# Optimization experiments

Measured on AMD Instinct MI355X. Metric: run time of the kernel, lower is better.

## Reference

```python
import jax, jax.numpy as jnp
import numpy as np

STRIDE = 4.0
NUM_CLASSES = 3
GH, GW = 40, 60
NBOX = 2 * GH * GW  # 4800
OBJ_CONF = 0.5
NMS_CONF = 0.4
# flattened anchor vector per cell after source's stack/transpose/tile/reshape:
# [wide_w, tall_w, wide_h, tall_h] (in grid units)
ANCH = jnp.array([60.0, 30.0, 20.0, 40.0], dtype=jnp.float32)


def _conv(x, w, b):
    y = jax.lax.conv_general_dilated(x, w, (1, 1), 'VALID',
                                     dimension_numbers=('NHWC', 'HWIO', 'NHWC'))
    return jax.nn.relu(y + b)


def _pool(x):
    return jax.lax.reduce_window(x, -jnp.inf, jax.lax.max,
                                 (1, 2, 2, 1), (1, 2, 2, 1), 'VALID')


def _predict_transform(p):
    # p: [B, GH, GW, 16]
    gx, gy = jnp.meshgrid(jnp.arange(GW, dtype=p.dtype), jnp.arange(GH, dtype=p.dtype))
    off = jnp.stack([gx, gy], axis=-1)  # [GH, GW, 2]
    xy1 = (jax.nn.sigmoid(p[..., 0:2]) + off) * STRIDE
    wh1 = jnp.exp(p[..., 2:4]) * ANCH[:2] * STRIDE
    conf1 = jax.nn.sigmoid(p[..., 4:5])
    cls1 = jax.nn.sigmoid(p[..., 5:8])
    xy2 = (p[..., 8:10] + off) * STRIDE          # source: no sigmoid on box2 xy
    wh2 = jnp.exp(p[..., 10:12]) * ANCH[2:4] * STRIDE
    conf2 = p[..., 12:13]                         # source: box2 conf never sigmoided
    cls2 = jax.nn.sigmoid(p[..., 13:16])
    return jnp.concatenate([xy1, wh1, conf1, cls1, xy2, wh2, conf2, cls2], axis=-1)


def _iou_one_vs_all(b, B):
    # b: [8], B: [N,8]; boxes are (cx, cy, w, h, ...). +1 pixel convention as in source.
    bx1, by1 = b[0] - b[2] / 2, b[1] - b[3] / 2
    bx2, by2 = b[0] + b[2] / 2, b[1] + b[3] / 2
    Bx1, By1 = B[:, 0] - B[:, 2] / 2, B[:, 1] - B[:, 3] / 2
    Bx2, By2 = B[:, 0] + B[:, 2] / 2, B[:, 1] + B[:, 3] / 2
    iw = jnp.clip(jnp.minimum(bx2, Bx2) - jnp.maximum(bx1, Bx1) + 1, 0)
    ih = jnp.clip(jnp.minimum(by2, By2) - jnp.maximum(by1, By1) + 1, 0)
    inter = iw * ih
    a1 = (bx2 - bx1 + 1) * (by2 - by1 + 1)
    a2 = (Bx2 - Bx1 + 1) * (By2 - By1 + 1)
    return inter / (a1 + a2 - inter)


def _nms_class(boxes, mask):
    # boxes: [N, 8], mask: [N] bool -> keep mask [N] bool in original order
    n = boxes.shape[0]
    score = jnp.where(mask, boxes[:, 4], -1.0)
    order = jnp.argsort(-score)               # confidence-descending
    bs = boxes[order]
    keep0 = mask[order]
    idx = jnp.arange(n)

    def body(i, keep):
        ious = _iou_one_vs_all(bs[i], bs)
        sup = (ious >= NMS_CONF) & (idx > i) & keep[i]
        return keep & ~sup

    keep = jax.lax.fori_loop(0, n, body, keep0)
    return jnp.zeros_like(mask).at[order].set(keep)


def _filter_boxes(pred_img):
    # pred_img: [GH, GW, 16] -> keep mask [NUM_CLASSES, NBOX]
    b1 = pred_img[..., :8].reshape(-1, 8)
    b2 = pred_img[..., 8:].reshape(-1, 8)
    boxes = jnp.concatenate([b1, b2], axis=0)  # [NBOX, 8]
    valid = boxes[:, 4] > OBJ_CONF
    cls_idx = jnp.argmax(boxes[:, 5:5 + NUM_CLASSES], axis=1)
    masks = valid[None, :] & (cls_idx[None, :] == jnp.arange(NUM_CLASSES)[:, None])
    return jax.vmap(lambda m: _nms_class(boxes, m))(masks)


def setup_inputs() -> dict:
    key = jax.random.key(0)
    ks = jax.random.split(key, 8)
    B = 8
    img = jax.random.normal(ks[0], (B, 160, 240, 3), dtype=jnp.float32)
    w1 = jax.random.normal(ks[1], (6, 6, 3, 32), dtype=jnp.float32) * 0.05
    b1 = jnp.zeros((32,), jnp.float32)
    w2 = jax.random.normal(ks[2], (3, 3, 32, 64), dtype=jnp.float32) * 0.05
    b2 = jnp.zeros((64,), jnp.float32)
    w3 = jax.random.normal(ks[3], (3, 3, 64, 128), dtype=jnp.float32) * 0.05
    b3 = jnp.zeros((128,), jnp.float32)
    F = 35 * 55 * 128  # flattened backbone features
    wd1 = jax.random.normal(ks[4], (F, 256), dtype=jnp.float32) * 0.01
    bd1 = jnp.zeros((256,), jnp.float32)
    wd2 = jax.random.normal(ks[5], (256, GH * GW * 16), dtype=jnp.float32) * 0.02
    bd2 = jnp.zeros((GH * GW * 16,), jnp.float32)
    return {'img': img, 'w1': w1, 'b1': b1, 'w2': w2, 'b2': b2, 'w3': w3, 'b3': b3,
            'wd1': wd1, 'bd1': bd1, 'wd2': wd2, 'bd2': bd2}


def reference(img, w1, b1, w2, b2, w3, b3, wd1, bd1, wd2, bd2):
    x = _conv(img, w1, b1)      # [B,155,235,32]
    x = _pool(x)                # [B,77,117,32]
    x = _conv(x, w2, b2)        # [B,75,115,64]
    x = _pool(x)                # [B,37,57,64]
    x = _conv(x, w3, b3)        # [B,35,55,128]
    x = x.reshape(x.shape[0], -1)
    x = jax.nn.relu(x @ wd1 + bd1)   # dropout is identity at inference
    x = x @ wd2 + bd2
    x = x.reshape(-1, GH, GW, 16)
    pred = _predict_transform(x)             # [B, GH, GW, 16]
    keep = jax.vmap(_filter_boxes)(pred)     # [B, NUM_CLASSES, NBOX] bool
    return pred, keep
```

## Files before the change

kernel.cpp:

```cpp
#include <hip/hip_runtime.h>
#include <stdint.h>


static __device__ __forceinline__ float sigmoidf_(float x) {
  return 1.0f / (1.0f + expf(-x));
}

__global__ __launch_bounds__(256) void k_conv1p(const float* __restrict__ in,
    const float* __restrict__ w, const float* __restrict__ bias, float* __restrict__ out) {
  __shared__ float s_in[21 * 37 * 3];
  __shared__ float s_w[6 * 6 * 3 * 32];
  int tx = blockIdx.x, ty = blockIdx.y, n = blockIdx.z;
  int tid = threadIdx.x;
  int iy0 = ty * 16, ix0 = tx * 32;
  for (int idx = tid; idx < 3456; idx += 256) s_w[idx] = w[idx];
  for (int idx = tid; idx < 21 * 37 * 3; idx += 256) {
    int c = idx % 3;
    int rem = idx / 3;
    int x = rem % 37, y = rem / 37;
    int gy = iy0 + y, gx = ix0 + x;
    float v = 0.f;
    if (gy < 160 && gx < 240) v = in[((size_t)(n * 160 + gy) * 240 + gx) * 3 + c];
    s_in[idx] = v;
  }
  __syncthreads();

  int cg = tid >> 6;
  int l = tid & 63;
  int py = l >> 2;
  int px0 = (l & 3) * 8;

  float acc[8][8];
  float bj[8];
#pragma unroll
  for (int j = 0; j < 8; j++) bj[j] = bias[cg * 8 + j];
#pragma unroll
  for (int k = 0; k < 8; k++)
#pragma unroll
    for (int j = 0; j < 8; j++) acc[k][j] = bj[j];

#pragma unroll 1
  for (int ky = 0; ky < 6; ky++) {
#pragma unroll 1
    for (int kx = 0; kx < 6; kx++) {
#pragma unroll 1
      for (int c = 0; c < 3; c++) {
        const float* ib = s_in + ((py + ky) * 37 + px0 + kx) * 3 + c;
        float iv[8];
#pragma unroll
        for (int k = 0; k < 8; k++) iv[k] = ib[k * 3];
        const float* wb = s_w + ((ky * 6 + kx) * 3 + c) * 32 + cg * 8;
        float wv[8];
#pragma unroll
        for (int j = 0; j < 8; j++) wv[j] = wb[j];
#pragma unroll
        for (int k = 0; k < 8; k++)
#pragma unroll
          for (int j = 0; j < 8; j++) acc[k][j] = fmaf(iv[k], wv[j], acc[k][j]);
      }
    }
  }
  float pm[4][8];
#pragma unroll
  for (int kk = 0; kk < 4; kk++)
#pragma unroll
    for (int j = 0; j < 8; j++) pm[kk][j] = fmaxf(acc[2 * kk][j], acc[2 * kk + 1][j]);
#pragma unroll
  for (int kk = 0; kk < 4; kk++)
#pragma unroll
    for (int j = 0; j < 8; j++) {
      float o = __shfl_down(pm[kk][j], 4);
      pm[kk][j] = fmaxf(pm[kk][j], o);
    }
  if (!(py & 1)) {
    int pyp = ty * 8 + (py >> 1);
    if (pyp < 77) {
#pragma unroll
      for (int kk = 0; kk < 4; kk++) {
        int pxp = tx * 16 + (l & 3) * 4 + kk;
        if (pxp < 117) {
          float* op = out + ((size_t)(n * 77 + pyp) * 117 + pxp) * 32 + cg * 8;
          float4 v0, v1;
          v0.x = fmaxf(pm[kk][0], 0.f); v0.y = fmaxf(pm[kk][1], 0.f);
          v0.z = fmaxf(pm[kk][2], 0.f); v0.w = fmaxf(pm[kk][3], 0.f);
          v1.x = fmaxf(pm[kk][4], 0.f); v1.y = fmaxf(pm[kk][5], 0.f);
          v1.z = fmaxf(pm[kk][6], 0.f); v1.w = fmaxf(pm[kk][7], 0.f);
          ((float4*)op)[0] = v0;
          ((float4*)op)[1] = v1;
        }
      }
    }
  }
}

__global__ __launch_bounds__(256) void k_conv2p(const float* __restrict__ in,
    const float* __restrict__ w, const float* __restrict__ bias, float* __restrict__ out) {
  __shared__ float s_in[32 * 10 * 18];
  int tx = blockIdx.x, ty = blockIdx.y, n = blockIdx.z;
  int tid = threadIdx.x;
  int iy0 = ty * 8, ix0 = tx * 16;
  for (int idx = tid; idx < 10 * 18 * 32; idx += 256) {
    int c = idx & 31;
    int rem = idx >> 5;
    int x = rem % 18, y = rem / 18;
    int gy = iy0 + y, gx = ix0 + x;
    float v = 0.f;
    if (gy < 77 && gx < 117) v = in[((size_t)(n * 77 + gy) * 117 + gx) * 32 + c];
    s_in[c * 180 + y * 18 + x] = v;
  }
  __syncthreads();

  int cg = tid >> 4;
  int pg = tid & 15;
  int py = pg >> 1;
  int px0 = (pg & 1) * 8;

  float acc[8][4];
  float bj[4];
#pragma unroll
  for (int j = 0; j < 4; j++) bj[j] = bias[cg * 4 + j];
#pragma unroll
  for (int k = 0; k < 8; k++)
#pragma unroll
    for (int j = 0; j < 4; j++) acc[k][j] = bj[j];

#pragma unroll 1
  for (int ky = 0; ky < 3; ky++) {
#pragma unroll 1
    for (int kx = 0; kx < 3; kx++) {
      const float* wbase = w + (size_t)((ky * 3 + kx) * 32) * 64 + cg * 4;
      const float* ibase = s_in + (py + ky) * 18 + px0 + kx;
#pragma unroll 4
      for (int c = 0; c < 32; c++) {
        float4 wa = *(const float4*)(wbase + (size_t)c * 64);
        const float* ib = ibase + c * 180;
        float iv[8];
#pragma unroll
        for (int k = 0; k < 8; k++) iv[k] = ib[k];
#pragma unroll
        for (int k = 0; k < 8; k++) {
          acc[k][0] = fmaf(iv[k], wa.x, acc[k][0]);
          acc[k][1] = fmaf(iv[k], wa.y, acc[k][1]);
          acc[k][2] = fmaf(iv[k], wa.z, acc[k][2]);
          acc[k][3] = fmaf(iv[k], wa.w, acc[k][3]);
        }
      }
    }
  }
  float pm[4][4];
#pragma unroll
  for (int kk = 0; kk < 4; kk++)
#pragma unroll
    for (int j = 0; j < 4; j++) pm[kk][j] = fmaxf(acc[2 * kk][j], acc[2 * kk + 1][j]);
#pragma unroll
  for (int kk = 0; kk < 4; kk++)
#pragma unroll
    for (int j = 0; j < 4; j++) {
      float o = __shfl_down(pm[kk][j], 2);
      pm[kk][j] = fmaxf(pm[kk][j], o);
    }
  if (!(pg & 2)) {
    int pyp = ty * 4 + (py >> 1);
    if (pyp < 37) {
#pragma unroll
      for (int kk = 0; kk < 4; kk++) {
        int pxp = tx * 8 + (pg & 1) * 4 + kk;
        if (pxp < 57) {
          float* op = out + ((size_t)(n * 37 + pyp) * 57 + pxp) * 64 + cg * 4;
          float4 v0;
          v0.x = fmaxf(pm[kk][0], 0.f); v0.y = fmaxf(pm[kk][1], 0.f);
          v0.z = fmaxf(pm[kk][2], 0.f); v0.w = fmaxf(pm[kk][3], 0.f);
          ((float4*)op)[0] = v0;
        }
      }
    }
  }
}

__global__ __launch_bounds__(256) void k_conv3(const float* __restrict__ in,
    const float* __restrict__ w, const float* __restrict__ bias, float* __restrict__ out) {
  __shared__ float s_in[64 * 6 * 18];
  int tx = blockIdx.x, ty = blockIdx.y, z = blockIdx.z;
  int n = z >> 1, h = z & 1;
  int tid = threadIdx.x;
  int iy0 = ty * 4, ix0 = tx * 16;
  for (int idx = tid; idx < 6 * 18 * 64; idx += 256) {
    int c = idx & 63;
    int rem = idx >> 6;
    int x = rem % 18, y = rem / 18;
    int gy = iy0 + y, gx = ix0 + x;
    float v = 0.f;
    if (gy < 37 && gx < 57) v = in[((size_t)(n * 37 + gy) * 57 + gx) * 64 + c];
    s_in[c * 108 + y * 18 + x] = v;
  }
  __syncthreads();

  int cg = tid >> 4;
  int pg = tid & 15;
  int py = pg >> 2;
  int px0 = (pg & 3) * 4;
  int ob = h * 64 + cg * 4;

  float acc[4][4];
  float bj[4];
#pragma unroll
  for (int j = 0; j < 4; j++) bj[j] = bias[ob + j];
#pragma unroll
  for (int k = 0; k < 4; k++)
#pragma unroll
    for (int j = 0; j < 4; j++) acc[k][j] = bj[j];

#pragma unroll 1
  for (int ky = 0; ky < 3; ky++) {
#pragma unroll 1
    for (int kx = 0; kx < 3; kx++) {
      const float* wbase = w + (size_t)((ky * 3 + kx) * 64) * 128 + ob;
      const float* ibase = s_in + (py + ky) * 18 + px0 + kx;
#pragma unroll 4
      for (int c = 0; c < 64; c++) {
        float4 wa = *(const float4*)(wbase + (size_t)c * 128);
        const float* ib = ibase + c * 108;
        float iv[4];
#pragma unroll
        for (int k = 0; k < 4; k++) iv[k] = ib[k];
#pragma unroll
        for (int k = 0; k < 4; k++) {
          acc[k][0] = fmaf(iv[k], wa.x, acc[k][0]);
          acc[k][1] = fmaf(iv[k], wa.y, acc[k][1]);
          acc[k][2] = fmaf(iv[k], wa.z, acc[k][2]);
          acc[k][3] = fmaf(iv[k], wa.w, acc[k][3]);
        }
      }
    }
  }
  int oy = iy0 + py;
  if (oy < 35) {
#pragma unroll
    for (int k = 0; k < 4; k++) {
      int ox = ix0 + px0 + k;
      if (ox < 55) {
        float* op = out + ((size_t)(n * 35 + oy) * 55 + ox) * 128 + ob;
        float4 v0;
        v0.x = fmaxf(acc[k][0], 0.f); v0.y = fmaxf(acc[k][1], 0.f);
        v0.z = fmaxf(acc[k][2], 0.f); v0.w = fmaxf(acc[k][3], 0.f);
        ((float4*)op)[0] = v0;
      }
    }
  }
}

__global__ __launch_bounds__(256) void k_dense1(const float* __restrict__ a3,
    const float* __restrict__ wd1, float* __restrict__ part) {
  __shared__ float red[4][64][33];
  __shared__ float s_x[256][8];
  int c = blockIdx.x;
  int tid = threadIdx.x;
  int c4 = tid & 63;
  int ks = tid >> 6;
  int k0 = c * 256;
  int kn = 246400 - k0;
  if (kn > 256) kn = 256;
  for (int idx = tid; idx < 2048; idx += 256) {
    int nn = idx >> 8, r = idx & 255;
    int rr = k0 + r;
    if (rr > 246399) rr = 246399;
    s_x[r][nn] = a3[(size_t)nn * 246400 + rr];
  }
  __syncthreads();
  float acc[8][4];
#pragma unroll
  for (int n = 0; n < 8; n++)
#pragma unroll
    for (int j = 0; j < 4; j++) acc[n][j] = 0.f;
  int kbeg = ks * 64;
  int kend = kbeg + 64;
  if (kend > kn) kend = kn;
#pragma unroll 8
  for (int kk = kbeg; kk < kend; kk++) {
    float4 wv = *(const float4*)(wd1 + (size_t)(k0 + kk) * 256 + c4 * 4);
    float4 xa = *(const float4*)&s_x[kk][0];
    float4 xb = *(const float4*)&s_x[kk][4];
    float xs[8] = {xa.x, xa.y, xa.z, xa.w, xb.x, xb.y, xb.z, xb.w};
#pragma unroll
    for (int n = 0; n < 8; n++) {
      acc[n][0] = fmaf(xs[n], wv.x, acc[n][0]);
      acc[n][1] = fmaf(xs[n], wv.y, acc[n][1]);
      acc[n][2] = fmaf(xs[n], wv.z, acc[n][2]);
      acc[n][3] = fmaf(xs[n], wv.w, acc[n][3]);
    }
  }
#pragma unroll
  for (int n = 0; n < 8; n++)
#pragma unroll
    for (int j = 0; j < 4; j++) red[ks][c4][n * 4 + j] = acc[n][j];
  __syncthreads();
  for (int o = tid; o < 2048; o += 256) {
    int col = o & 255, n = o >> 8;
    int cc = col >> 2, j = col & 3;
    float s = red[0][cc][n * 4 + j] + red[1][cc][n * 4 + j] +
              red[2][cc][n * 4 + j] + red[3][cc][n * 4 + j];
    part[(size_t)c * 2048 + n * 256 + col] = s;
  }
}

__global__ __launch_bounds__(256) void k_reduce1a(const float* __restrict__ part,
    float* __restrict__ partr) {
  int bx = blockIdx.x;
  int t = blockIdx.y * 256 + threadIdx.x;
  int cbeg = bx * 61;
  int cend = cbeg + 61;
  if (cend > 963) cend = 963;
  float s = 0.f;
#pragma unroll 4
  for (int c = cbeg; c < cend; c++) s += part[(size_t)c * 2048 + t];
  partr[(size_t)bx * 2048 + t] = s;
}

__global__ __launch_bounds__(256) void k_dense2t(const float* __restrict__ partr,
    const float* __restrict__ bd1, const float* __restrict__ wd2,
    const float* __restrict__ bd2, float* __restrict__ pred,
    float4* __restrict__ boxd4, float* __restrict__ meta) {
  __shared__ float red[8][32][33];
  __shared__ float s_d1[256][8];
  int jb = blockIdx.x;
  int tid = threadIdx.x;
  for (int idx = tid; idx < 2048; idx += 256) {
    int n = idx >> 8, j = idx & 255;
    float s = 0.f;
#pragma unroll
    for (int b = 0; b < 16; b++) s += partr[b * 2048 + idx];
    s_d1[j][n] = fmaxf(s + bd1[j], 0.f);
  }
  __syncthreads();
  int c4 = tid & 31;
  int ks = tid >> 5;
  int j0 = jb * 128 + c4 * 4;
  float acc[8][4];
#pragma unroll
  for (int n = 0; n < 8; n++)
#pragma unroll
    for (int j = 0; j < 4; j++) acc[n][j] = 0.f;
#pragma unroll 4
  for (int kk = 0; kk < 32; kk++) {
    int row = ks * 32 + kk;
    float4 wv = *(const float4*)(wd2 + (size_t)row * 38400 + j0);
    float4 xa = *(const float4*)&s_d1[row][0];
    float4 xb = *(const float4*)&s_d1[row][4];
    float xs[8] = {xa.x, xa.y, xa.z, xa.w, xb.x, xb.y, xb.z, xb.w};
#pragma unroll
    for (int n = 0; n < 8; n++) {
      acc[n][0] = fmaf(xs[n], wv.x, acc[n][0]);
      acc[n][1] = fmaf(xs[n], wv.y, acc[n][1]);
      acc[n][2] = fmaf(xs[n], wv.z, acc[n][2]);
      acc[n][3] = fmaf(xs[n], wv.w, acc[n][3]);
    }
  }
#pragma unroll
  for (int n = 0; n < 8; n++)
#pragma unroll
    for (int j = 0; j < 4; j++) red[ks][c4][n * 4 + j] = acc[n][j];
  __syncthreads();
  if (tid >= 64) return;
  int n = tid >> 3, cc = tid & 7;
  int cell = jb * 8 + cc;
  float v[16];
#pragma unroll
  for (int q = 0; q < 16; q++) {
    int lc = cc * 16 + q;
    int cq = lc >> 2, jq = lc & 3;
    float s = 0.f;
#pragma unroll
    for (int g = 0; g < 8; g++) s += red[g][cq][n * 4 + jq];
    v[q] = s + bd2[jb * 128 + lc];
  }
  float gx = (float)(cell % 60), gy = (float)(cell / 60);
  float o[16];
  o[0] = (sigmoidf_(v[0]) + gx) * 4.0f;
  o[1] = (sigmoidf_(v[1]) + gy) * 4.0f;
  o[2] = expf(v[2]) * 60.0f * 4.0f;
  o[3] = expf(v[3]) * 30.0f * 4.0f;
  o[4] = sigmoidf_(v[4]);
  o[5] = sigmoidf_(v[5]);
  o[6] = sigmoidf_(v[6]);
  o[7] = sigmoidf_(v[7]);
  o[8] = (v[8] + gx) * 4.0f;
  o[9] = (v[9] + gy) * 4.0f;
  o[10] = expf(v[10]) * 20.0f * 4.0f;
  o[11] = expf(v[11]) * 40.0f * 4.0f;
  o[12] = v[12];
  o[13] = sigmoidf_(v[13]);
  o[14] = sigmoidf_(v[14]);
  o[15] = sigmoidf_(v[15]);
  float* op = pred + ((size_t)n * 2400 + cell) * 16;
#pragma unroll
  for (int q4 = 0; q4 < 4; q4++) {
    float4 w4;
    w4.x = o[q4 * 4 + 0]; w4.y = o[q4 * 4 + 1];
    w4.z = o[q4 * 4 + 2]; w4.w = o[q4 * 4 + 3];
    ((float4*)op)[q4] = w4;
  }
#pragma unroll
  for (int h = 0; h < 2; h++) {
    int b = n * 4800 + h * 2400 + cell;
    float X = o[h * 8 + 0], Y = o[h * 8 + 1], W = o[h * 8 + 2], H = o[h * 8 + 3];
    float conf = o[h * 8 + 4];
    float c0 = o[h * 8 + 5], c1 = o[h * 8 + 6], c2 = o[h * 8 + 7];
    int cls = 0; float best = c0;
    if (c1 > best) { best = c1; cls = 1; }
    if (c2 > best) { best = c2; cls = 2; }
    float x1 = X - W / 2.0f, y1 = Y - H / 2.0f;
    float x2 = X + W / 2.0f, y2 = Y + H / 2.0f;
    boxd4[b] = make_float4(x1, y1, x2, y2);
    meta[2 * b] = conf;
    ((int*)meta)[2 * b + 1] = cls;
  }
}

__global__ __launch_bounds__(256) void k_nms_sort(const float4* __restrict__ boxd4,
    const float* __restrict__ meta, int* __restrict__ cnt,
    float4* __restrict__ sbf, int* __restrict__ sidx, float* __restrict__ keep_out) {
  __shared__ unsigned long long key[8192];
  __shared__ int scnt;
  int bid = blockIdx.x;
  int n = bid / 3, c = bid - n * 3;
  int tid = threadIdx.x;
  float* ko = keep_out + (size_t)bid * 4800;
  for (int s = tid; s < 4800; s += 256) ko[s] = 0.f;
  if (tid == 0) scnt = 0;
  __syncthreads();

  const float* mt = meta + (size_t)n * 9600;
  for (int p = tid; p < 4800; p += 256) {
    float2 m = ((const float2*)mt)[p];
    float conf = m.x;
    int cls = __float_as_int(m.y);
    if (conf > 0.5f && cls == c) {
      int slot = atomicAdd(&scnt, 1);
      unsigned u = __float_as_uint(conf);
      unsigned asc = (u & 0x80000000u) ? ~u : (u | 0x80000000u);
      key[slot] = (((unsigned long long)(~asc)) << 32) | (unsigned)p;
    }
  }
  __syncthreads();
  int V = scnt;
  if (tid == 0) cnt[bid] = V;
  if (V == 0) return;
  int Vp2 = 1;
  while (Vp2 < V) Vp2 <<= 1;
  for (int s = V + tid; s < Vp2; s += 256) key[s] = ~0ull;

  for (int k = 2; k <= Vp2; k <<= 1) {
    for (int j = k >> 1; j > 0; j >>= 1) {
      __syncthreads();
      int jm = j - 1;
      for (int t2 = tid; t2 < (Vp2 >> 1); t2 += 256) {
        int i = ((t2 & ~jm) << 1) | (t2 & jm);
        int q = i | j;
        bool up = ((i & k) == 0);
        unsigned long long a = key[i], b2 = key[q];
        if ((a > b2) == up) { key[i] = b2; key[q] = a; }
      }
    }
  }
  __syncthreads();
  float4* sb = sbf + (size_t)bid * 4800;
  int* si = sidx + (size_t)bid * 4800;
  const float4* bsrc = boxd4 + (size_t)n * 4800;
  for (int s = tid; s < V; s += 256) {
    unsigned p = (unsigned)(key[s] & 0xFFFFFFFFull);
    sb[s] = bsrc[p];
    si[s] = (int)p;
  }
}

__global__ __launch_bounds__(256) void k_iou_mat(const int* __restrict__ cnt,
    const float4* __restrict__ sbf, unsigned long long* __restrict__ mat) {
  int nc = blockIdx.x;
  int w = blockIdx.y;
  int V = cnt[nc];
  if (V == 0 || V > 1024) return;
  int W = (V + 63) >> 6;
  if (w >= W) return;
  int tid = threadIdx.x;
  int l = tid & 63, wv = tid >> 6;
  const float4* sb = sbf + (size_t)nc * 4800;
  int col = (w << 6) + l;
  float4 bj = sb[col < V ? col : (V - 1)];
  float aj = (bj.z - bj.x + 1.0f) * (bj.w - bj.y + 1.0f);
  unsigned long long* mrow = mat + (size_t)nc * 1024 * 16 + w;
  for (int i = wv; i < V; i += 4) {
    float4 bi = sb[i];
    float iw = fminf(bi.z, bj.z) - fmaxf(bi.x, bj.x) + 1.0f;
    float ih = fminf(bi.w, bj.w) - fmaxf(bi.y, bj.y) + 1.0f;
    iw = fmaxf(iw, 0.f);
    ih = fmaxf(ih, 0.f);
    float inter = iw * ih;
    float ai = (bi.z - bi.x + 1.0f) * (bi.w - bi.y + 1.0f);
    float iou = inter / (ai + aj - inter);
    bool pr = (col > i) && (col < V) && (iou >= 0.4f);
    unsigned long long word = __ballot(pr);
    if (l == 0) mrow[(size_t)i * 16] = word;
  }
}

__global__ __launch_bounds__(256) void k_nms_scan(const int* __restrict__ cnt,
    const unsigned long long* __restrict__ mat, const float4* __restrict__ sbf,
    const int* __restrict__ sidx, float* __restrict__ keep_out) {
  __shared__ float4 sbL[4800];
  __shared__ unsigned long long avail[75];
  int nc = blockIdx.x;
  int V = cnt[nc];
  if (V == 0) return;
  int tid = threadIdx.x;
  float* ko = keep_out + (size_t)nc * 4800;
  const int* si = sidx + (size_t)nc * 4800;

  if (V <= 1024) {
    if (tid >= 64) return;
    int l = tid;
    int W = (V + 63) >> 6;
    const unsigned long long* mbase = mat + (size_t)nc * 1024 * 16;
    bool act = (l < W);
    unsigned long long av = 0ull;
    if (act) {
      int rem = V - (l << 6);
      av = (rem >= 64) ? ~0ull : ((1ull << rem) - 1ull);
    }
    unsigned long long mA[16], mB[16];
#pragma unroll
    for (int k = 0; k < 16; k++)
      mA[k] = (act && k < V) ? mbase[(size_t)k * 16 + l] : 0ull;
    for (int i0 = 0; i0 < V; i0 += 16) {
      int nx = i0 + 16;
#pragma unroll
      for (int k = 0; k < 16; k++)
        mB[k] = (act && (nx + k) < V) ? mbase[(size_t)(nx + k) * 16 + l] : 0ull;
      int wi = i0 >> 6;
      unsigned long long mloc[16];
#pragma unroll
      for (int k = 0; k < 16; k++) mloc[k] = __shfl(mA[k], wi, 64);
      unsigned long long cur = __shfl(av, wi, 64);
      unsigned alive = 0;
#pragma unroll
      for (int k = 0; k < 16; k++) {
        int i = i0 + k;
        if (i < V && ((cur >> (i & 63)) & 1ull)) {
          alive |= 1u << k;
          cur &= ~mloc[k];
        }
      }
#pragma unroll
      for (int k = 0; k < 16; k++)
        if ((alive >> k) & 1u) av &= ~mA[k];
      if (l < 16 && ((alive >> l) & 1u) && (i0 + l) < V) ko[si[i0 + l]] = 1.0f;
#pragma unroll
      for (int k = 0; k < 16; k++) mA[k] = mB[k];
    }
    return;
  }

  {
    const float4* sb = sbf + (size_t)nc * 4800;
    for (int s = tid; s < V; s += 256) sbL[s] = sb[s];
    for (int w = tid; w < 75; w += 256) {
      int rem = V - (w << 6);
      avail[w] = (rem >= 64) ? ~0ull : (rem <= 0 ? 0ull : ((1ull << rem) - 1ull));
    }
    __syncthreads();
    if (tid >= 64) return;
    int l = tid;
    int wlast = (V - 1) >> 6;
    for (;;) {
      int cand = 0x7FFFFFFF;
      unsigned long long a0 = avail[l];
      if (a0) cand = (l << 6) + __ffsll((long long)a0) - 1;
      if (l < 11) {
        unsigned long long a1 = avail[64 + l];
        if (a1) {
          int c2 = ((64 + l) << 6) + __ffsll((long long)a1) - 1;
          if (c2 < cand) cand = c2;
        }
      }
#pragma unroll
      for (int off = 32; off > 0; off >>= 1) {
        int o = __shfl_xor(cand, off, 64);
        if (o < cand) cand = o;
      }
      if (cand == 0x7FFFFFFF) break;
      int i = cand;
      int tw = i >> 6;
      if (l == 0) {
        ko[si[i]] = 1.0f;
        avail[tw] &= ~(1ull << (i & 63));
      }
      float4 bi = sbL[i];
      float ai = (bi.z - bi.x + 1.0f) * (bi.w - bi.y + 1.0f);
      for (int w = tw; w <= wlast; w++) {
        unsigned long long aw = avail[w];
        if (!aw) continue;
        int col = (w << 6) + l;
        float4 bj = sbL[col];
        float iw = fminf(bi.z, bj.z) - fmaxf(bi.x, bj.x) + 1.0f;
        float ih = fminf(bi.w, bj.w) - fmaxf(bi.y, bj.y) + 1.0f;
        iw = fmaxf(iw, 0.f);
        ih = fmaxf(ih, 0.f);
        float inter = iw * ih;
        float aj = (bj.z - bj.x + 1.0f) * (bj.w - bj.y + 1.0f);
        float iou = inter / (ai + aj - inter);
        bool pr = (col > i) && (col < V) && (iou >= 0.4f);
        unsigned long long word = __ballot(pr);
        if (word && l == 0) avail[w] = aw & ~word;
      }
    }
  }
}

extern "C" void kernel_launch(void* const* d_in, const int* in_sizes, int n_in,
                              void* d_out, int out_size, void* d_ws, size_t ws_size,
                              hipStream_t stream) {
  const float* img = (const float*)d_in[0];
  const float* w1 = (const float*)d_in[1];
  const float* b1 = (const float*)d_in[2];
  const float* w2 = (const float*)d_in[3];
  const float* b2 = (const float*)d_in[4];
  const float* w3 = (const float*)d_in[5];
  const float* b3 = (const float*)d_in[6];
  const float* wd1 = (const float*)d_in[7];
  const float* bd1 = (const float*)d_in[8];
  const float* wd2 = (const float*)d_in[9];
  const float* bd2 = (const float*)d_in[10];

  float* ws = (float*)d_ws;
  float* a3 = ws + 0;
  float* pd1 = ws + 3942400;
  float* partr = ws + 5914624;
  float4* boxd4 = (float4*)(ws + 5947392);
  float* meta = ws + 6100992;
  float4* sbf = (float4*)(ws + 6177792);
  int* sidx = (int*)(ws + 6638592);
  int* cnt = (int*)(ws + 6753792);
  float* p1 = ws + 9324800;
  float* p2 = ws + 16047104;
  unsigned long long* mat = (unsigned long long*)(ws + 3942400);

  float* pred = (float*)d_out;
  float* keep = pred + 307200;

  k_conv1p<<<dim3(8, 10, 8), 256, 0, stream>>>(img, w1, b1, p1);
  k_conv2p<<<dim3(8, 10, 8), 256, 0, stream>>>(p1, w2, b2, p2);
  k_conv3<<<dim3(4, 9, 16), 256, 0, stream>>>(p2, w3, b3, a3);
  k_dense1<<<963, 256, 0, stream>>>(a3, wd1, pd1);
  k_reduce1a<<<dim3(16, 8), 256, 0, stream>>>(pd1, partr);
  k_dense2t<<<300, 256, 0, stream>>>(partr, bd1, wd2, bd2, pred, boxd4, meta);
  k_nms_sort<<<24, 256, 0, stream>>>(boxd4, meta, cnt, sbf, sidx, keep);
  k_iou_mat<<<dim3(24, 16), 256, 0, stream>>>(cnt, sbf, mat);
  k_nms_scan<<<24, 256, 0, stream>>>(cnt, mat, sbf, sidx, keep);
}
```

Before: 358.8 us.

## Split conv and dense1 work across more blocks with smaller per-thread tiles

Each conv kernel now uses smaller per-thread or per-block output tiles and launches more blocks. conv1 splits its output channels into two halves along the z grid axis, while conv2 and conv3 halve the spatial tile width. dense1 drops the in-block split-K reduction through shared memory: each thread now owns one batch row and four columns across the full 256-length K chunk, with the column range split across two grid rows. The aim is more parallelism and occupancy on a GPU with many CUs, at the cost of more redundant input and halo loads and lower register reuse per FMA.

```diff
diff --git a/kernel.cpp b/kernel.cpp
--- a/kernel.cpp
+++ b/kernel.cpp
@@ -9,11 +9,15 @@
 __global__ __launch_bounds__(256) void k_conv1p(const float* __restrict__ in,
     const float* __restrict__ w, const float* __restrict__ bias, float* __restrict__ out) {
   __shared__ float s_in[21 * 37 * 3];
-  __shared__ float s_w[6 * 6 * 3 * 32];
-  int tx = blockIdx.x, ty = blockIdx.y, n = blockIdx.z;
+  __shared__ float s_w[6 * 6 * 3 * 16];
+  int tx = blockIdx.x, ty = blockIdx.y, z = blockIdx.z;
+  int n = z >> 1, h = z & 1;
   int tid = threadIdx.x;
   int iy0 = ty * 16, ix0 = tx * 32;
-  for (int idx = tid; idx < 3456; idx += 256) s_w[idx] = w[idx];
+  for (int idx = tid; idx < 1728; idx += 256) {
+    int q = idx >> 4, o = idx & 15;
+    s_w[idx] = w[q * 32 + h * 16 + o];
+  }
   for (int idx = tid; idx < 21 * 37 * 3; idx += 256) {
     int c = idx % 3;
     int rem = idx / 3;
@@ -29,15 +33,16 @@
   int l = tid & 63;
   int py = l >> 2;
   int px0 = (l & 3) * 8;
-
-  float acc[8][8];
-  float bj[8];
-#pragma unroll
-  for (int j = 0; j < 8; j++) bj[j] = bias[cg * 8 + j];
+  int ob = h * 16 + cg * 4;
+
+  float acc[8][4];
+  float bj[4];
+#pragma unroll
+  for (int j = 0; j < 4; j++) bj[j] = bias[ob + j];
 #pragma unroll
   for (int k = 0; k < 8; k++)
 #pragma unroll
-    for (int j = 0; j < 8; j++) acc[k][j] = bj[j];
+    for (int j = 0; j < 4; j++) acc[k][j] = bj[j];
 
 #pragma unroll 1
   for (int ky = 0; ky < 6; ky++) {
@@ -49,26 +54,26 @@
         float iv[8];
 #pragma unroll
         for (int k = 0; k < 8; k++) iv[k] = ib[k * 3];
-        const float* wb = s_w + ((ky * 6 + kx) * 3 + c) * 32 + cg * 8;
-        float wv[8];
-#pragma unroll
-        for (int j = 0; j < 8; j++) wv[j] = wb[j];
+        const float* wb = s_w + ((ky * 6 + kx) * 3 + c) * 16 + cg * 4;
+        float wv[4];
+#pragma unroll
+        for (int j = 0; j < 4; j++) wv[j] = wb[j];
 #pragma unroll
         for (int k = 0; k < 8; k++)
 #pragma unroll
-          for (int j = 0; j < 8; j++) acc[k][j] = fmaf(iv[k], wv[j], acc[k][j]);
-      }
-    }
-  }
-  float pm[4][8];
+          for (int j = 0; j < 4; j++) acc[k][j] = fmaf(iv[k], wv[j], acc[k][j]);
+      }
+    }
+  }
+  float pm[4][4];
 #pragma unroll
   for (int kk = 0; kk < 4; kk++)
 #pragma unroll
-    for (int j = 0; j < 8; j++) pm[kk][j] = fmaxf(acc[2 * kk][j], acc[2 * kk + 1][j]);
+    for (int j = 0; j < 4; j++) pm[kk][j] = fmaxf(acc[2 * kk][j], acc[2 * kk + 1][j]);
 #pragma unroll
   for (int kk = 0; kk < 4; kk++)
 #pragma unroll
-    for (int j = 0; j < 8; j++) {
+    for (int j = 0; j < 4; j++) {
       float o = __shfl_down(pm[kk][j], 4);
       pm[kk][j] = fmaxf(pm[kk][j], o);
     }
@@ -79,14 +84,11 @@
       for (int kk = 0; kk < 4; kk++) {
         int pxp = tx * 16 + (l & 3) * 4 + kk;
         if (pxp < 117) {
-          float* op = out + ((size_t)(n * 77 + pyp) * 117 + pxp) * 32 + cg * 8;
-          float4 v0, v1;
+          float* op = out + ((size_t)(n * 77 + pyp) * 117 + pxp) * 32 + ob;
+          float4 v0;
           v0.x = fmaxf(pm[kk][0], 0.f); v0.y = fmaxf(pm[kk][1], 0.f);
           v0.z = fmaxf(pm[kk][2], 0.f); v0.w = fmaxf(pm[kk][3], 0.f);
-          v1.x = fmaxf(pm[kk][4], 0.f); v1.y = fmaxf(pm[kk][5], 0.f);
-          v1.z = fmaxf(pm[kk][6], 0.f); v1.w = fmaxf(pm[kk][7], 0.f);
           ((float4*)op)[0] = v0;
-          ((float4*)op)[1] = v1;
         }
       }
     }
@@ -95,32 +97,32 @@
 
 __global__ __launch_bounds__(256) void k_conv2p(const float* __restrict__ in,
     const float* __restrict__ w, const float* __restrict__ bias, float* __restrict__ out) {
-  __shared__ float s_in[32 * 10 * 18];
+  __shared__ float s_in[32 * 10 * 10];
   int tx = blockIdx.x, ty = blockIdx.y, n = blockIdx.z;
   int tid = threadIdx.x;
-  int iy0 = ty * 8, ix0 = tx * 16;
-  for (int idx = tid; idx < 10 * 18 * 32; idx += 256) {
+  int iy0 = ty * 8, ix0 = tx * 8;
+  for (int idx = tid; idx < 10 * 10 * 32; idx += 256) {
     int c = idx & 31;
     int rem = idx >> 5;
-    int x = rem % 18, y = rem / 18;
+    int x = rem % 10, y = rem / 10;
     int gy = iy0 + y, gx = ix0 + x;
     float v = 0.f;
     if (gy < 77 && gx < 117) v = in[((size_t)(n * 77 + gy) * 117 + gx) * 32 + c];
-    s_in[c * 180 + y * 18 + x] = v;
+    s_in[c * 100 + y * 10 + x] = v;
   }
   __syncthreads();
 
   int cg = tid >> 4;
   int pg = tid & 15;
   int py = pg >> 1;
-  int px0 = (pg & 1) * 8;
-
-  float acc[8][4];
+  int px0 = (pg & 1) * 4;
+
+  float acc[4][4];
   float bj[4];
 #pragma unroll
   for (int j = 0; j < 4; j++) bj[j] = bias[cg * 4 + j];
 #pragma unroll
-  for (int k = 0; k < 8; k++)
+  for (int k = 0; k < 4; k++)
 #pragma unroll
     for (int j = 0; j < 4; j++) acc[k][j] = bj[j];
 
@@ -129,16 +131,16 @@
 #pragma unroll 1
     for (int kx = 0; kx < 3; kx++) {
       const float* wbase = w + (size_t)((ky * 3 + kx) * 32) * 64 + cg * 4;
-      const float* ibase = s_in + (py + ky) * 18 + px0 + kx;
+      const float* ibase = s_in + (py + ky) * 10 + px0 + kx;
 #pragma unroll 4
       for (int c = 0; c < 32; c++) {
         float4 wa = *(const float4*)(wbase + (size_t)c * 64);
-        const float* ib = ibase + c * 180;
-        float iv[8];
-#pragma unroll
-        for (int k = 0; k < 8; k++) iv[k] = ib[k];
-#pragma unroll
-        for (int k = 0; k < 8; k++) {
+        const float* ib = ibase + c * 100;
+        float iv[4];
+#pragma unroll
+        for (int k = 0; k < 4; k++) iv[k] = ib[k];
+#pragma unroll
+        for (int k = 0; k < 4; k++) {
           acc[k][0] = fmaf(iv[k], wa.x, acc[k][0]);
           acc[k][1] = fmaf(iv[k], wa.y, acc[k][1]);
           acc[k][2] = fmaf(iv[k], wa.z, acc[k][2]);
@@ -147,13 +149,13 @@
       }
     }
   }
-  float pm[4][4];
-#pragma unroll
-  for (int kk = 0; kk < 4; kk++)
+  float pm[2][4];
+#pragma unroll
+  for (int kk = 0; kk < 2; kk++)
 #pragma unroll
     for (int j = 0; j < 4; j++) pm[kk][j] = fmaxf(acc[2 * kk][j], acc[2 * kk + 1][j]);
 #pragma unroll
-  for (int kk = 0; kk < 4; kk++)
+  for (int kk = 0; kk < 2; kk++)
 #pragma unroll
     for (int j = 0; j < 4; j++) {
       float o = __shfl_down(pm[kk][j], 2);
@@ -163,8 +165,8 @@
     int pyp = ty * 4 + (py >> 1);
     if (pyp < 37) {
 #pragma unroll
-      for (int kk = 0; kk < 4; kk++) {
-        int pxp = tx * 8 + (pg & 1) * 4 + kk;
+      for (int kk = 0; kk < 2; kk++) {
+        int pxp = tx * 4 + (pg & 1) * 2 + kk;
         if (pxp < 57) {
           float* op = out + ((size_t)(n * 37 + pyp) * 57 + pxp) * 64 + cg * 4;
           float4 v0;
@@ -179,34 +181,34 @@
 
 __global__ __launch_bounds__(256) void k_conv3(const float* __restrict__ in,
     const float* __restrict__ w, const float* __restrict__ bias, float* __restrict__ out) {
-  __shared__ float s_in[64 * 6 * 18];
+  __shared__ float s_in[64 * 6 * 10];
   int tx = blockIdx.x, ty = blockIdx.y, z = blockIdx.z;
   int n = z >> 1, h = z & 1;
   int tid = threadIdx.x;
-  int iy0 = ty * 4, ix0 = tx * 16;
-  for (int idx = tid; idx < 6 * 18 * 64; idx += 256) {
+  int iy0 = ty * 4, ix0 = tx * 8;
+  for (int idx = tid; idx < 6 * 10 * 64; idx += 256) {
     int c = idx & 63;
     int rem = idx >> 6;
-    int x = rem % 18, y = rem / 18;
+    int x = rem % 10, y = rem / 10;
     int gy = iy0 + y, gx = ix0 + x;
     float v = 0.f;
     if (gy < 37 && gx < 57) v = in[((size_t)(n * 37 + gy) * 57 + gx) * 64 + c];
-    s_in[c * 108 + y * 18 + x] = v;
+    s_in[c * 60 + y * 10 + x] = v;
   }
   __syncthreads();
 
   int cg = tid >> 4;
   int pg = tid & 15;
   int py = pg >> 2;
-  int px0 = (pg & 3) * 4;
+  int px0 = (pg & 3) * 2;
   int ob = h * 64 + cg * 4;
 
-  float acc[4][4];
+  float acc[2][4];
   float bj[4];
 #pragma unroll
   for (int j = 0; j < 4; j++) bj[j] = bias[ob + j];
 #pragma unroll
-  for (int k = 0; k < 4; k++)
+  for (int k = 0; k < 2; k++)
 #pragma unroll
     for (int j = 0; j < 4; j++) acc[k][j] = bj[j];
 
@@ -215,16 +217,16 @@
 #pragma unroll 1
     for (int kx = 0; kx < 3; kx++) {
       const float* wbase = w + (size_t)((ky * 3 + kx) * 64) * 128 + ob;
-      const float* ibase = s_in + (py + ky) * 18 + px0 + kx;
+      const float* ibase = s_in + (py + ky) * 10 + px0 + kx;
 #pragma unroll 4
       for (int c = 0; c < 64; c++) {
         float4 wa = *(const float4*)(wbase + (size_t)c * 128);
-        const float* ib = ibase + c * 108;
-        float iv[4];
-#pragma unroll
-        for (int k = 0; k < 4; k++) iv[k] = ib[k];
-#pragma unroll
-        for (int k = 0; k < 4; k++) {
+        const float* ib = ibase + c * 60;
+        float iv[2];
+        iv[0] = ib[0];
+        iv[1] = ib[1];
+#pragma unroll
+        for (int k = 0; k < 2; k++) {
           acc[k][0] = fmaf(iv[k], wa.x, acc[k][0]);
           acc[k][1] = fmaf(iv[k], wa.y, acc[k][1]);
           acc[k][2] = fmaf(iv[k], wa.z, acc[k][2]);
@@ -236,7 +238,7 @@
   int oy = iy0 + py;
   if (oy < 35) {
 #pragma unroll
-    for (int k = 0; k < 4; k++) {
+    for (int k = 0; k < 2; k++) {
       int ox = ix0 + px0 + k;
       if (ox < 55) {
         float* op = out + ((size_t)(n * 35 + oy) * 55 + ox) * 128 + ob;
@@ -251,12 +253,10 @@
 
 __global__ __launch_bounds__(256) void k_dense1(const float* __restrict__ a3,
     const float* __restrict__ wd1, float* __restrict__ part) {
-  __shared__ float red[4][64][33];
   __shared__ float s_x[256][8];
   int c = blockIdx.x;
-  int tid = threadIdx.x;
-  int c4 = tid & 63;
-  int ks = tid >> 6;
+  int half = blockIdx.y;
+  int tid = threadIdx.x;
   int k0 = c * 256;
   int kn = 246400 - k0;
   if (kn > 256) kn = 256;
@@ -267,40 +267,21 @@
     s_x[r][nn] = a3[(size_t)nn * 246400 + rr];
   }
   __syncthreads();
-  float acc[8][4];
-#pragma unroll
-  for (int n = 0; n < 8; n++)
-#pragma unroll
-    for (int j = 0; j < 4; j++) acc[n][j] = 0.f;
-  int kbeg = ks * 64;
-  int kend = kbeg + 64;
-  if (kend > kn) kend = kn;
+  int n = tid >> 5;
+  int c4 = tid & 31;
+  int col = half * 128 + c4 * 4;
+  float acc0 = 0.f, acc1 = 0.f, acc2 = 0.f, acc3 = 0.f;
+  const float* wp = wd1 + (size_t)k0 * 256 + col;
 #pragma unroll 8
-  for (int kk = kbeg; kk < kend; kk++) {
-    float4 wv = *(const float4*)(wd1 + (size_t)(k0 + kk) * 256 + c4 * 4);
-    float4 xa = *(const float4*)&s_x[kk][0];
-    float4 xb = *(const float4*)&s_x[kk][4];
-    float xs[8] = {xa.x, xa.y, xa.z, xa.w, xb.x, xb.y, xb.z, xb.w};
-#pragma unroll
-    for (int n = 0; n < 8; n++) {
-      acc[n][0] = fmaf(xs[n], wv.x, acc[n][0]);
-      acc[n][1] = fmaf(xs[n], wv.y, acc[n][1]);
-      acc[n][2] = fmaf(xs[n], wv.z, acc[n][2]);
-      acc[n][3] = fmaf(xs[n], wv.w, acc[n][3]);
-    }
-  }
-#pragma unroll
-  for (int n = 0; n < 8; n++)
-#pragma unroll
-    for (int j = 0; j < 4; j++) red[ks][c4][n * 4 + j] = acc[n][j];
-  __syncthreads();
-  for (int o = tid; o < 2048; o += 256) {
-    int col = o & 255, n = o >> 8;
-    int cc = col >> 2, j = col & 3;
-    float s = red[0][cc][n * 4 + j] + red[1][cc][n * 4 + j] +
-              red[2][cc][n * 4 + j] + red[3][cc][n * 4 + j];
-    part[(size_t)c * 2048 + n * 256 + col] = s;
-  }
+  for (int kk = 0; kk < kn; kk++) {
+    float4 wv = *(const float4*)(wp + (size_t)kk * 256);
+    float x = s_x[kk][n];
+    acc0 = fmaf(x, wv.x, acc0);
+    acc1 = fmaf(x, wv.y, acc1);
+    acc2 = fmaf(x, wv.z, acc2);
+    acc3 = fmaf(x, wv.w, acc3);
+  }
+  *(float4*)(part + (size_t)c * 2048 + n * 256 + col) = make_float4(acc0, acc1, acc2, acc3);
 }
 
 __global__ __launch_bounds__(256) void k_reduce1a(const float* __restrict__ part,
@@ -646,10 +627,11 @@
   float* pred = (float*)d_out;
   float* keep = pred + 307200;
 
-  k_conv1p<<<dim3(8, 10, 8), 256, 0, stream>>>(img, w1, b1, p1);
-  k_conv2p<<<dim3(8, 10, 8), 256, 0, stream>>>(p1, w2, b2, p2);
-  k_conv3<<<dim3(4, 9, 16), 256, 0, stream>>>(p2, w3, b3, a3);
-  k_dense1<<<963, 256, 0, stream>>>(a3, wd1, pd1);
+  k_conv1p<<<dim3(8, 10, 16), 256, 0, stream>>>(img, w1, b1, p1);
+  k_conv2p<<<dim3(15, 10, 8), 256, 0, stream>>>(p1, w2, b2, p2);
+  k_conv3<<<dim3(7, 9, 16), 256, 0, stream>>>(p2, w3, b3, a3);
+  dim3 gd1(963, 2);
+  k_dense1<<<gd1, 256, 0, stream>>>(a3, wd1, pd1);
   k_reduce1a<<<dim3(16, 8), 256, 0, stream>>>(pd1, partr);
   k_dense2t<<<300, 256, 0, stream>>>(partr, bd1, wd2, bd2, pred, boxd4, meta);
   k_nms_sort<<<24, 256, 0, stream>>>(boxd4, meta, cnt, sbf, sidx, keep);
```

Measured after the change: 402.1 us. +12.1%, slower.
